# Optimization experiments

Hardware: AMD Instinct MI355X
Metric: run time of the kernel (lower is better)

## Reference

```python
import jax, jax.numpy as jnp
import numpy as np

EPS = 1e-5

def binarize(x):
    # sign binarization with straight-through estimator (matches .data replacement in torch BNN code)
    s = jnp.where(x >= 0, 1.0, -1.0).astype(x.dtype)
    return x + jax.lax.stop_gradient(s - x)

def conv3x3(x, w):
    return jax.lax.conv_general_dilated(x, w, (1, 1), ((1, 1), (1, 1)),
                                        dimension_numbers=('NCHW', 'OIHW', 'NCHW'))

def bn4(x, g, b, m, v):
    inv = jax.lax.rsqrt(v + EPS)
    return (x - m[None, :, None, None]) * (g * inv)[None, :, None, None] + b[None, :, None, None]

def bn2(x, g, b, m, v):
    return (x - m) * (g * jax.lax.rsqrt(v + EPS)) + b

def maxpool2(x):
    return jax.lax.reduce_window(x, -jnp.inf, jax.lax.max, (1, 1, 2, 2), (1, 1, 2, 2), 'VALID')

def ht(x):
    return jnp.clip(x, -1.0, 1.0)


def setup_inputs() -> dict:
    key = jax.random.key(0)
    ks = iter(jax.random.split(key, 64))
    d = {}
    d['x'] = jax.random.normal(next(ks), (256, 3, 32, 32), jnp.float32)
    conv_shapes = [(128, 3), (128, 128), (256, 128), (256, 256), (512, 256), (512, 512)]
    for i, (co, ci) in enumerate(conv_shapes, start=1):
        d[f'w{i}'] = jax.random.normal(next(ks), (co, ci, 3, 3), jnp.float32) * 0.05
        d[f'g{i}'] = jax.random.uniform(next(ks), (co,), jnp.float32, 0.5, 1.5)
        d[f'b{i}'] = jax.random.normal(next(ks), (co,), jnp.float32) * 0.1
        d[f'm{i}'] = jax.random.normal(next(ks), (co,), jnp.float32) * 0.1
        d[f'v{i}'] = jax.random.uniform(next(ks), (co,), jnp.float32, 0.5, 1.5)
    d['bias2'] = jax.random.normal(next(ks), (128,), jnp.float32) * 0.1  # conv2 has default bias=True
    fc_shapes = [(1024, 512 * 4 * 4), (1024, 1024), (10, 1024)]
    for j, (co, ci) in enumerate(fc_shapes, start=7):
        d[f'w{j}'] = jax.random.normal(next(ks), (co, ci), jnp.float32) * 0.02
        d[f'm{j}'] = jax.random.normal(next(ks), (co,), jnp.float32) * 0.1
        d[f'v{j}'] = jax.random.uniform(next(ks), (co,), jnp.float32, 0.5, 1.5)
        if j < 9:  # last BN is affine=False
            d[f'g{j}'] = jax.random.uniform(next(ks), (co,), jnp.float32, 0.5, 1.5)
            d[f'b{j}'] = jax.random.normal(next(ks), (co,), jnp.float32) * 0.1
    return d


def reference(x, w1, g1, b1, m1, v1, w2, bias2, g2, b2, m2, v2, w3, g3, b3, m3, v3,
              w4, g4, b4, m4, v4, w5, g5, b5, m5, v5, w6, g6, b6, m6, v6,
              w7, g7, b7, m7, v7, w8, g8, b8, m8, v8, w9, m9, v9):
    # features
    h = conv3x3(x, binarize(w1))                      # first layer: input NOT binarized (3 channels)
    h = ht(bn4(h, g1, b1, m1, v1))
    h = conv3x3(binarize(h), binarize(w2)) + bias2[None, :, None, None]
    h = ht(bn4(maxpool2(h), g2, b2, m2, v2))
    h = conv3x3(binarize(h), binarize(w3))
    h = ht(bn4(h, g3, b3, m3, v3))
    h = conv3x3(binarize(h), binarize(w4))
    h = ht(bn4(maxpool2(h), g4, b4, m4, v4))
    h = conv3x3(binarize(h), binarize(w5))
    h = ht(bn4(h, g5, b5, m5, v5))
    h = conv3x3(binarize(h), binarize(w6))
    h = ht(bn4(maxpool2(h), g6, b6, m6, v6))          # [B, 512, 4, 4]
    # classifier
    h = h.reshape(-1, 512 * 4 * 4)
    h = ht(bn2(binarize(h) @ binarize(w7).T, g7, b7, m7, v7))
    h = ht(bn2(binarize(h) @ binarize(w8).T, g8, b8, m8, v8))
    h = binarize(h) @ binarize(w9).T
    h = (h - m9) * jax.lax.rsqrt(v9 + EPS)            # BatchNorm1d(affine=False)
    return jax.nn.log_softmax(h, axis=-1)
```

## Files before the change

kernel.cpp:

```cpp
#include <hip/hip_runtime.h>
#include <stdint.h>

typedef unsigned long long u64;

static __device__ __forceinline__ int uread(int v) { return __builtin_amdgcn_readfirstlane(v); }
static __device__ __forceinline__ float fr(float x) { __asm__ volatile("" : "+v"(x)); return x; }

static __device__ __forceinline__ bool bn_neg(float x, float g, float b, float m, float v) {
    float inv = fr(1.0f / fr(sqrtf(fr(v + 1e-5f))));
    float si  = fr(g * inv);
    float t1  = fr(x - m);
    float t2  = fr(t1 * si);
    float bn  = fr(t2 + b);
    return bn < 0.0f;
}


__global__ __launch_bounds__(256) void packw1_kernel(const float* __restrict__ w, float* __restrict__ ws) {
    int id = blockIdx.x * 256 + threadIdx.x;
    if (id >= 27 * 128) return;
    int co = id & 127, j = id >> 7;
    ws[j * 128 + co] = (w[co * 27 + j] < 0.f) ? -1.f : 1.f;
}

__global__ __launch_bounds__(256) void packw_conv2_kernel(const float* __restrict__ w, u64* __restrict__ wb,
                                                          int CINW, int COUT) {
    int wv = blockIdx.x * 4 + (threadIdx.x >> 6);
    if (wv >= COUT * CINW) return;
    int lane = threadIdx.x & 63;
    int wrd = wv % CINW, co = wv / CINW;
    int CIN = CINW * 64;
    const float* p = w + ((size_t)co * CIN + (size_t)wrd * 64 + lane) * 9;
    float f[9];
#pragma unroll
    for (int t = 0; t < 9; ++t) f[t] = p[t];
#pragma unroll
    for (int t = 0; t < 9; ++t) {
        u64 bits = __ballot(f[t] < 0.f);
        if (lane == 0) wb[(size_t)(t * CINW + wrd) * COUT + co] = bits;
    }
}

__global__ __launch_bounds__(256) void packw7_kernel(const float* __restrict__ w, u64* __restrict__ wb) {
    int wv = blockIdx.x * 4 + (threadIdx.x >> 6);
    if (wv >= 1024 * 8) return;
    int lane = threadIdx.x & 63;
    int cw = wv & 7, o = wv >> 3;
    const float* p = w + (size_t)o * 8192 + (size_t)(cw * 64 + lane) * 16;
    float f[16];
#pragma unroll
    for (int i = 0; i < 16; i += 4) {
        float4 q = *(const float4*)(p + i);
        f[i] = q.x; f[i + 1] = q.y; f[i + 2] = q.z; f[i + 3] = q.w;
    }
#pragma unroll
    for (int pixel = 0; pixel < 16; ++pixel) {
        u64 bits = __ballot(f[pixel] < 0.f);
        if (lane == 0) wb[(size_t)(pixel * 8 + cw) * 1024 + o] = bits;
    }
}

__global__ __launch_bounds__(256) void packw8_kernel(const float* __restrict__ w, u64* __restrict__ wb) {
    int wv = blockIdx.x * 4 + (threadIdx.x >> 6);
    if (wv >= 1024 * 16) return;
    int lane = threadIdx.x & 63;
    int k = wv & 15, o = wv >> 4;
    float f = w[(size_t)o * 1024 + k * 64 + lane];
    u64 bits = __ballot(f < 0.f);
    if (lane == 0) wb[(size_t)k * 1024 + o] = bits;
}

__global__ __launch_bounds__(256) void packw9_kernel(const float* __restrict__ w, u64* __restrict__ wb) {
    int wv = blockIdx.x * 4 + (threadIdx.x >> 6);
    if (wv >= 160) return;
    int lane = threadIdx.x & 63;
    int k = wv & 15, o = wv >> 4;
    float f = w[(size_t)o * 1024 + k * 64 + lane];
    u64 bits = __ballot(f < 0.f);
    if (lane == 0) wb[k * 16 + o] = bits;
}

__global__ __launch_bounds__(256, 4) void conv1_kernel(
    const float* __restrict__ x, const float* __restrict__ w1s,
    const float* __restrict__ g, const float* __restrict__ bb,
    const float* __restrict__ m, const float* __restrict__ v,
    u64* __restrict__ out, int N)
{
    int lane = threadIdx.x & 63;
    int rid = uread(blockIdx.x * 4 + (threadIdx.x >> 6));
    if (rid >= N * 32) return;
    int n = rid >> 5, y = rid & 31;
    const float* xb = x + (size_t)n * 3072;
    const bool rv0 = (y > 0), rv2 = (y < 31);
    const int y0 = rv0 ? y - 1 : 0, y2 = rv2 ? y + 1 : 31;

    int co0 = lane, co1 = 64 + lane;
    float w0[27], w1[27];
#pragma unroll
    for (int j = 0; j < 27; ++j) {
        w0[j] = fr(w1s[j * 128 + co0]);
        w1[j] = fr(w1s[j * 128 + co1]);
    }
    float g0 = g[co0], b0 = bb[co0], m0 = m[co0], v0 = v[co0];
    float g1 = g[co1], b1 = bb[co1], m1 = m[co1], v1 = v[co1];

    float cm[9], cc[9], cn[9];
#pragma unroll
    for (int t = 0; t < 9; ++t) cm[t] = 0.f;

    auto ldcol = [&](float* c, int xs) {
#pragma unroll
        for (int ci = 0; ci < 3; ++ci) {
            float a0 = xb[ci * 1024 + y0 * 32 + xs];
            float a1 = xb[ci * 1024 + y  * 32 + xs];
            float a2 = xb[ci * 1024 + y2 * 32 + xs];
            c[0 + ci] = fr(rv0 ? a0 : 0.f);
            c[3 + ci] = fr(a1);
            c[6 + ci] = fr(rv2 ? a2 : 0.f);
        }
    };
    ldcol(cc, 0);

    u64* orow = out + (((size_t)n * 32 + y) * 32) * 2;

    for (int xx = 0; xx < 32; ++xx) {
        if (xx < 31) ldcol(cn, xx + 1);
        else {
#pragma unroll
            for (int t = 0; t < 9; ++t) cn[t] = 0.f;
        }
        float a0 = 0.f, a1 = 0.f;
#pragma unroll
        for (int ky = 0; ky < 3; ++ky) {
#pragma unroll
            for (int ci = 0; ci < 3; ++ci) a0 = fmaf(w0[ci * 9 + ky * 3 + 0], cm[ky * 3 + ci], a0);
#pragma unroll
            for (int ci = 0; ci < 3; ++ci) a0 = fmaf(w0[ci * 9 + ky * 3 + 1], cc[ky * 3 + ci], a0);
#pragma unroll
            for (int ci = 0; ci < 3; ++ci) a0 = fmaf(w0[ci * 9 + ky * 3 + 2], cn[ky * 3 + ci], a0);
        }
#pragma unroll
        for (int ky = 0; ky < 3; ++ky) {
#pragma unroll
            for (int ci = 0; ci < 3; ++ci) a1 = fmaf(w1[ci * 9 + ky * 3 + 0], cm[ky * 3 + ci], a1);
#pragma unroll
            for (int ci = 0; ci < 3; ++ci) a1 = fmaf(w1[ci * 9 + ky * 3 + 1], cc[ky * 3 + ci], a1);
#pragma unroll
            for (int ci = 0; ci < 3; ++ci) a1 = fmaf(w1[ci * 9 + ky * 3 + 2], cn[ky * 3 + ci], a1);
        }
        u64 bits0 = __ballot(bn_neg(a0, g0, b0, m0, v0));
        u64 bits1 = __ballot(bn_neg(a1, g1, b1, m1, v1));
        if (lane == 0) {
            ulonglong2 st; st.x = bits0; st.y = bits1;
            *(ulonglong2*)(orow + xx * 2) = st;
        }
#pragma unroll
        for (int t = 0; t < 9; ++t) { cm[t] = cc[t]; cc[t] = cn[t]; }
    }
}

template<int WORDS, int COW, bool POOL, bool HAS_BIAS, int H, int YS, int MINW>
__global__ __launch_bounds__(256, MINW) void binconv_lds(
    const u64* __restrict__ a, const u64* __restrict__ wb,
    const float* __restrict__ g, const float* __restrict__ bb,
    const float* __restrict__ m, const float* __restrict__ v,
    const float* __restrict__ bias, u64* __restrict__ out, int N)
{
    const int W = H;
    const int OH = POOL ? H / 2 : H, OW = POOL ? W / 2 : W;
    const int COUT = COW * 64;
    const int OROWS = OH / YS;
    const int RMAX = POOL ? OROWS * 2 + 2 : OROWS + 2;
    const int PR = POOL ? 4 : 3;
    const int NW = POOL ? 4 : 1;
    const int W2 = WORDS / 2;
    const int S = POOL ? 2 : 1;
    const int NBC = 9 * WORDS * 64;

    __shared__ alignas(16) u64 tile[RMAX * W * WORDS];

    int blk = blockIdx.x;
    int ys = blk % YS, n = blk / YS;
    int oy0 = ys * OROWS;
    int iy0 = (POOL ? oy0 * 2 - 1 : oy0 - 1); if (iy0 < 0) iy0 = 0;
    int iy1 = (POOL ? (oy0 + OROWS - 1) * 2 + 2 : oy0 + OROWS); if (iy1 > H - 1) iy1 = H - 1;
    int R = iy1 - iy0 + 1;
    {
        const u64* src = a + ((size_t)(n * H + iy0) * W) * WORDS;
        int tot = R * W * WORDS;
        for (int i = threadIdx.x; i < tot; i += 256) tile[i] = src[i];
    }
    __syncthreads();

    int lane = threadIdx.x & 63;
    int wv = uread((int)(threadIdx.x >> 6));

    int cw0, r0, r1;
    if (COW >= 4) { cw0 = wv; r0 = 0; r1 = OROWS; }
    else { cw0 = wv % COW; int chunk = OROWS * COW / 4; r0 = (wv / COW) * chunk; r1 = r0 + chunk; }

    const ulonglong2* t2 = (const ulonglong2*)tile;

    for (int cw = cw0; cw < COW; cw += 4) {
        int co = cw * 64 + lane;
        u64 wgt[9 * WORDS];
#pragma unroll
        for (int t = 0; t < 9 * WORDS; ++t) wgt[t] = wb[(size_t)t * COUT + co];
        float gc = g[co], bc = bb[co], mc = m[co], vc = v[co];
        float bi = HAS_BIAS ? bias[co] : 0.f;

        auto store_px = [&](int oy, int ox, int best) {
            float tv = (float)best;
            if (HAS_BIAS) tv = fr(tv + bi);
            u64 bits = __ballot(bn_neg(tv, gc, bc, mc, vc));
            if (lane == 0) out[((size_t)(n * OH + oy) * OW + ox) * COW + cw] = bits;
        };

        auto px_general = [&](int oy, int ox) {
            int y0 = (POOL ? oy * 2 : oy) - 1;
            bool rv[PR];
#pragma unroll
            for (int p = 0; p < PR; ++p) rv[p] = ((unsigned)(y0 + p) < (unsigned)H);
            int x0 = (POOL ? ox * 2 : ox) - 1;
            bool cv[PR];
#pragma unroll
            for (int q = 0; q < PR; ++q) cv[q] = ((unsigned)(x0 + q) < (unsigned)W);

            int acc[NW], nb[NW];
#pragma unroll
            for (int i = 0; i < NW; ++i) { acc[i] = 0; nb[i] = 0; }
#pragma unroll
            for (int sy = 0; sy < (POOL ? 2 : 1); ++sy)
#pragma unroll
            for (int sx = 0; sx < (POOL ? 2 : 1); ++sx)
#pragma unroll
            for (int ky = 0; ky < 3; ++ky)
#pragma unroll
            for (int kx = 0; kx < 3; ++kx)
                if (rv[sy + ky] && cv[sx + kx]) nb[POOL ? sy * 2 + sx : 0] += WORDS * 64;

#pragma unroll
            for (int w2 = 0; w2 < W2; ++w2) {
                ulonglong2 pt[PR][PR];
#pragma unroll
                for (int p = 0; p < PR; ++p) if (rv[p]) {
                    int lrow = y0 + p - iy0;
#pragma unroll
                    for (int q = 0; q < PR; ++q) if (cv[q])
                        pt[p][q] = t2[(lrow * W + (x0 + q)) * W2 + w2];
                }
#pragma unroll
                for (int sy = 0; sy < (POOL ? 2 : 1); ++sy)
#pragma unroll
                for (int sx = 0; sx < (POOL ? 2 : 1); ++sx)
#pragma unroll
                for (int ky = 0; ky < 3; ++ky)
#pragma unroll
                for (int kx = 0; kx < 3; ++kx)
                    if (rv[sy + ky] && cv[sx + kx]) {
                        ulonglong2 q = pt[sy + ky][sx + kx];
                        int wi = POOL ? sy * 2 + sx : 0;
                        acc[wi] += __popcll(q.x ^ wgt[(ky * 3 + kx) * WORDS + 2 * w2])
                                 + __popcll(q.y ^ wgt[(ky * 3 + kx) * WORDS + 2 * w2 + 1]);
                    }
            }
            int best = 0;
#pragma unroll
            for (int i = 0; i < NW; ++i) {
                int dot = nb[i] - 2 * acc[i];
                best = (i == 0) ? dot : max(best, dot);
            }
            store_px(oy, ox, best);
        };

        for (int oy = oy0 + r0; oy < oy0 + r1; ++oy) {
            int y0 = (POOL ? oy * 2 : oy) - 1;
            if (y0 < 0 || y0 + PR > H) {
                for (int ox = 0; ox < OW; ++ox) px_general(oy, ox);
                continue;
            }
            int base = y0 - iy0;
            px_general(oy, 0);
            if constexpr (W2 == 1) {
                ulonglong2 win[PR][PR];
                const int xl = POOL ? 1 : 0;
#pragma unroll
                for (int p = 0; p < PR; ++p)
#pragma unroll
                    for (int q = 0; q < PR; ++q)
                        win[p][q] = t2[(base + p) * W + xl + q];
                for (int ox = 1; ox < OW - 1; ++ox) {
                    int acc[NW];
#pragma unroll
                    for (int i = 0; i < NW; ++i) acc[i] = 0;
#pragma unroll
                    for (int sy = 0; sy < (POOL ? 2 : 1); ++sy)
#pragma unroll
                    for (int sx = 0; sx < (POOL ? 2 : 1); ++sx)
#pragma unroll
                    for (int ky = 0; ky < 3; ++ky)
#pragma unroll
                    for (int kx = 0; kx < 3; ++kx) {
                        ulonglong2 q = win[sy + ky][sx + kx];
                        int wi = POOL ? sy * 2 + sx : 0;
                        acc[wi] += __popcll(q.x ^ wgt[(ky * 3 + kx) * WORDS])
                                 + __popcll(q.y ^ wgt[(ky * 3 + kx) * WORDS + 1]);
                    }
                    int best = 0;
#pragma unroll
                    for (int i = 0; i < NW; ++i) {
                        int dot = NBC - 2 * acc[i];
                        best = (i == 0) ? dot : max(best, dot);
                    }
                    store_px(oy, ox, best);
                    if (ox < OW - 2) {
                        int xnew = (POOL ? ox * 2 - 1 : ox - 1) + PR;
#pragma unroll
                        for (int p = 0; p < PR; ++p) {
#pragma unroll
                            for (int q = 0; q < PR - S; ++q) win[p][q] = win[p][q + S];
#pragma unroll
                            for (int s = 0; s < S; ++s)
                                win[p][PR - S + s] = t2[(base + p) * W + xnew + s];
                        }
                    }
                }
            } else {
                for (int ox = 1; ox < OW - 1; ++ox) {
                    int x0 = (POOL ? ox * 2 : ox) - 1;
                    int acc[NW];
#pragma unroll
                    for (int i = 0; i < NW; ++i) acc[i] = 0;
#pragma unroll
                    for (int w2 = 0; w2 < W2; ++w2) {
                        ulonglong2 pt[PR][PR];
#pragma unroll
                        for (int p = 0; p < PR; ++p)
#pragma unroll
                            for (int q = 0; q < PR; ++q)
                                pt[p][q] = t2[((base + p) * W + (x0 + q)) * W2 + w2];
#pragma unroll
                        for (int sy = 0; sy < (POOL ? 2 : 1); ++sy)
#pragma unroll
                        for (int sx = 0; sx < (POOL ? 2 : 1); ++sx)
#pragma unroll
                        for (int ky = 0; ky < 3; ++ky)
#pragma unroll
                        for (int kx = 0; kx < 3; ++kx) {
                            ulonglong2 q = pt[sy + ky][sx + kx];
                            int wi = POOL ? sy * 2 + sx : 0;
                            acc[wi] += __popcll(q.x ^ wgt[(ky * 3 + kx) * WORDS + 2 * w2])
                                     + __popcll(q.y ^ wgt[(ky * 3 + kx) * WORDS + 2 * w2 + 1]);
                        }
                    }
                    int best = 0;
#pragma unroll
                    for (int i = 0; i < NW; ++i) {
                        int dot = NBC - 2 * acc[i];
                        best = (i == 0) ? dot : max(best, dot);
                    }
                    store_px(oy, ox, best);
                }
            }
            px_general(oy, OW - 1);
        }
    }
}

template<int KW, int OWRD>
__global__ __launch_bounds__(256) void binfc_kernel(
    const u64* __restrict__ a, const u64* __restrict__ wb,
    const float* __restrict__ g, const float* __restrict__ bb,
    const float* __restrict__ m, const float* __restrict__ v,
    u64* __restrict__ out, int N)
{
    int lane = threadIdx.x & 63;
    int wid = uread(blockIdx.x * 4 + (threadIdx.x >> 6));
    if (wid >= N * OWRD) return;
    int ow = wid & (OWRD - 1), n = wid / OWRD;
    int o = ow * 64 + lane;
    const u64* ap = a + (size_t)n * KW;
    int acc = 0;
#pragma unroll 8
    for (int k = 0; k < KW; ++k)
        acc += __popcll(ap[k] ^ wb[(size_t)k * (OWRD * 64) + o]);
    float dotf = (float)(KW * 64 - 2 * acc);
    u64 bits = __ballot(bn_neg(dotf, g[o], bb[o], m[o], v[o]));
    if (lane == 0) out[(size_t)n * OWRD + ow] = bits;
}

__global__ __launch_bounds__(64) void fc9_kernel(
    const u64* __restrict__ a, const u64* __restrict__ wb,
    const float* __restrict__ m, const float* __restrict__ v, float* __restrict__ out)
{
    int n = blockIdx.x, t = threadIdx.x;
    const u64* ap = a + (size_t)n * 16;
    float val = -1e30f;
    if (t < 10) {
        int acc = 0;
#pragma unroll
        for (int k = 0; k < 16; ++k) acc += __popcll(ap[k] ^ wb[k * 16 + t]);
        float dotf = (float)(1024 - 2 * acc);
        float inv = fr(1.0f / fr(sqrtf(fr(v[t] + 1e-5f))));
        float t1  = fr(dotf - m[t]);
        val = fr(t1 * inv);
    }
    float mx = val;
#pragma unroll
    for (int off = 32; off; off >>= 1) mx = fmaxf(mx, __shfl_xor(mx, off));
    float sh = fr(val - mx);
    double e = (t < 10) ? exp((double)sh) : 0.0;
    double sum = e;
#pragma unroll
    for (int off = 32; off; off >>= 1) sum += __shfl_xor(sum, off);
    if (t < 10) out[n * 10 + t] = (float)((double)sh - log(sum));
}

extern "C" void kernel_launch(void* const* d_in, const int* in_sizes, int n_in,
                              void* d_out, int out_size, void* d_ws, size_t ws_size,
                              hipStream_t stream) {
    auto F = [&](int i) { return (const float*)d_in[i]; };
    const float* x  = F(0);
    const float* w1 = F(1);  const float* g1 = F(2);  const float* b1 = F(3);
    const float* m1 = F(4);  const float* v1 = F(5);
    const float* w2 = F(6);  const float* g2 = F(7);  const float* b2 = F(8);
    const float* m2 = F(9);  const float* v2 = F(10);
    const float* w3 = F(11); const float* g3 = F(12); const float* b3 = F(13);
    const float* m3 = F(14); const float* v3 = F(15);
    const float* w4 = F(16); const float* g4 = F(17); const float* b4 = F(18);
    const float* m4 = F(19); const float* v4 = F(20);
    const float* w5 = F(21); const float* g5 = F(22); const float* b5 = F(23);
    const float* m5 = F(24); const float* v5 = F(25);
    const float* w6 = F(26); const float* g6 = F(27); const float* b6 = F(28);
    const float* m6 = F(29); const float* v6 = F(30);
    const float* bias2 = F(31);
    const float* w7 = F(32); const float* m7 = F(33); const float* v7 = F(34);
    const float* g7 = F(35); const float* b7 = F(36);
    const float* w8 = F(37); const float* m8 = F(38); const float* v8 = F(39);
    const float* g8 = F(40); const float* b8 = F(41);
    const float* w9 = F(42); const float* m9 = F(43); const float* v9 = F(44);
    (void)in_sizes; (void)n_in; (void)ws_size;

    const int N = out_size / 10;
    u64* ws = (u64*)d_ws;
    size_t off = 0;
    auto carve = [&](size_t nwords) { u64* p = ws + off; off += nwords; return p; };
    float* w1s = (float*)carve(1728);
    u64* w2p = carve(2304);
    u64* w3p = carve(4608);
    u64* w4p = carve(9216);
    u64* w5p = carve(18432);
    u64* w6p = carve(36864);
    u64* w7p = carve(131072);
    u64* w8p = carve(16384);
    u64* w9p = carve(256);
    u64* a1 = carve((size_t)N * 32 * 32 * 2);
    u64* a2 = carve((size_t)N * 16 * 16 * 2);
    u64* a3 = carve((size_t)N * 16 * 16 * 4);
    u64* a4 = carve((size_t)N * 8 * 8 * 4);
    u64* a5 = carve((size_t)N * 8 * 8 * 8);
    u64* a6 = carve((size_t)N * 16 * 8);
    u64* f7 = carve((size_t)N * 16);
    u64* f8 = carve((size_t)N * 16);

    packw1_kernel<<<(3456 + 255) / 256, 256, 0, stream>>>(w1, w1s);
    packw_conv2_kernel<<<(128 * 2 + 3) / 4, 256, 0, stream>>>(w2, w2p, 2, 128);
    packw_conv2_kernel<<<(256 * 2 + 3) / 4, 256, 0, stream>>>(w3, w3p, 2, 256);
    packw_conv2_kernel<<<(256 * 4 + 3) / 4, 256, 0, stream>>>(w4, w4p, 4, 256);
    packw_conv2_kernel<<<(512 * 4 + 3) / 4, 256, 0, stream>>>(w5, w5p, 4, 512);
    packw_conv2_kernel<<<(512 * 8 + 3) / 4, 256, 0, stream>>>(w6, w6p, 8, 512);
    packw7_kernel<<<(8192 + 3) / 4, 256, 0, stream>>>(w7, w7p);
    packw8_kernel<<<(16384 + 3) / 4, 256, 0, stream>>>(w8, w8p);
    packw9_kernel<<<(160 + 3) / 4, 256, 0, stream>>>(w9, w9p);

    conv1_kernel<<<(N * 32 + 3) / 4, 256, 0, stream>>>(x, w1s, g1, b1, m1, v1, a1, N);

    binconv_lds<2, 2, true, true, 32, 4, 3><<<N * 4, 256, 0, stream>>>(
        a1, w2p, g2, b2, m2, v2, bias2, a2, N);
    binconv_lds<2, 4, false, false, 16, 4, 3><<<N * 4, 256, 0, stream>>>(
        a2, w3p, g3, b3, m3, v3, nullptr, a3, N);
    binconv_lds<4, 4, true, false, 16, 4, 2><<<N * 4, 256, 0, stream>>>(
        a3, w4p, g4, b4, m4, v4, nullptr, a4, N);
    binconv_lds<4, 8, false, false, 8, 4, 2><<<N * 4, 256, 0, stream>>>(
        a4, w5p, g5, b5, m5, v5, nullptr, a5, N);
    binconv_lds<8, 8, true, false, 8, 4, 2><<<N * 4, 256, 0, stream>>>(
        a5, w6p, g6, b6, m6, v6, nullptr, a6, N);

    binfc_kernel<128, 16><<<(N * 16 + 3) / 4, 256, 0, stream>>>(a6, w7p, g7, b7, m7, v7, f7, N);
    binfc_kernel<16, 16><<<(N * 16 + 3) / 4, 256, 0, stream>>>(f7, w8p, g8, b8, m8, v8, f8, N);

    fc9_kernel<<<N, 64, 0, stream>>>(f8, w9p, m9, v9, (float*)d_out);
}
```

Measured before the change: 703.0 us.

## Stream weight chunks per word-pair and reuse sliding windows in wide binconv layers

For the binary conv layers with more than two 64-bit words per pixel, the kernel no longer holds all 9*WORDS weight words in registers. It loops over word pairs, loading 18 weights per chunk and accumulating groups of output pixels along the row with a sliding window loaded from LDS. This lowers register pressure, so the launch-bounds occupancy hint is raised for conv4, conv5 and conv6. The cost is that weights are reloaded from global memory once per pixel group and word pair.

```diff
diff --git a/kernel.cpp b/kernel.cpp
--- a/kernel.cpp
+++ b/kernel.cpp
@@ -176,6 +176,8 @@
     const int W2 = WORDS / 2;
     const int S = POOL ? 2 : 1;
     const int NBC = 9 * WORDS * 64;
+    const int GPX = (OW <= 4) ? OW : ((NW == 4) ? 4 : OW);
+    const int NG = OW / GPX;
 
     __shared__ alignas(16) u64 tile[RMAX * W * WORDS];
 
@@ -203,9 +205,6 @@
 
     for (int cw = cw0; cw < COW; cw += 4) {
         int co = cw * 64 + lane;
-        u64 wgt[9 * WORDS];
-#pragma unroll
-        for (int t = 0; t < 9 * WORDS; ++t) wgt[t] = wb[(size_t)t * COUT + co];
         float gc = g[co], bc = bb[co], mc = m[co], vc = v[co];
         float bi = HAS_BIAS ? bias[co] : 0.f;
 
@@ -216,38 +215,41 @@
             if (lane == 0) out[((size_t)(n * OH + oy) * OW + ox) * COW + cw] = bits;
         };
 
-        auto px_general = [&](int oy, int ox) {
-            int y0 = (POOL ? oy * 2 : oy) - 1;
-            bool rv[PR];
-#pragma unroll
-            for (int p = 0; p < PR; ++p) rv[p] = ((unsigned)(y0 + p) < (unsigned)H);
-            int x0 = (POOL ? ox * 2 : ox) - 1;
-            bool cv[PR];
-#pragma unroll
-            for (int q = 0; q < PR; ++q) cv[q] = ((unsigned)(x0 + q) < (unsigned)W);
-
-            int acc[NW], nb[NW];
-#pragma unroll
-            for (int i = 0; i < NW; ++i) { acc[i] = 0; nb[i] = 0; }
-#pragma unroll
-            for (int sy = 0; sy < (POOL ? 2 : 1); ++sy)
-#pragma unroll
-            for (int sx = 0; sx < (POOL ? 2 : 1); ++sx)
-#pragma unroll
-            for (int ky = 0; ky < 3; ++ky)
-#pragma unroll
-            for (int kx = 0; kx < 3; ++kx)
-                if (rv[sy + ky] && cv[sx + kx]) nb[POOL ? sy * 2 + sx : 0] += WORDS * 64;
-
-#pragma unroll
-            for (int w2 = 0; w2 < W2; ++w2) {
+        if constexpr (W2 == 1) {
+            u64 wgt[18];
+#pragma unroll
+            for (int t = 0; t < 18; ++t) wgt[t] = wb[(size_t)t * COUT + co];
+
+            auto px_general = [&](int oy, int ox) {
+                int y0 = (POOL ? oy * 2 : oy) - 1;
+                bool rv[PR];
+#pragma unroll
+                for (int p = 0; p < PR; ++p) rv[p] = ((unsigned)(y0 + p) < (unsigned)H);
+                int x0 = (POOL ? ox * 2 : ox) - 1;
+                bool cv[PR];
+#pragma unroll
+                for (int q = 0; q < PR; ++q) cv[q] = ((unsigned)(x0 + q) < (unsigned)W);
+
+                int acc[NW], nb[NW];
+#pragma unroll
+                for (int i = 0; i < NW; ++i) { acc[i] = 0; nb[i] = 0; }
+#pragma unroll
+                for (int sy = 0; sy < (POOL ? 2 : 1); ++sy)
+#pragma unroll
+                for (int sx = 0; sx < (POOL ? 2 : 1); ++sx)
+#pragma unroll
+                for (int ky = 0; ky < 3; ++ky)
+#pragma unroll
+                for (int kx = 0; kx < 3; ++kx)
+                    if (rv[sy + ky] && cv[sx + kx]) nb[POOL ? sy * 2 + sx : 0] += WORDS * 64;
+
                 ulonglong2 pt[PR][PR];
 #pragma unroll
                 for (int p = 0; p < PR; ++p) if (rv[p]) {
                     int lrow = y0 + p - iy0;
 #pragma unroll
                     for (int q = 0; q < PR; ++q) if (cv[q])
-                        pt[p][q] = t2[(lrow * W + (x0 + q)) * W2 + w2];
+                        pt[p][q] = t2[(lrow * W + (x0 + q))];
                 }
 #pragma unroll
                 for (int sy = 0; sy < (POOL ? 2 : 1); ++sy)
@@ -260,28 +262,26 @@
                     if (rv[sy + ky] && cv[sx + kx]) {
                         ulonglong2 q = pt[sy + ky][sx + kx];
                         int wi = POOL ? sy * 2 + sx : 0;
-                        acc[wi] += __popcll(q.x ^ wgt[(ky * 3 + kx) * WORDS + 2 * w2])
-                                 + __popcll(q.y ^ wgt[(ky * 3 + kx) * WORDS + 2 * w2 + 1]);
+                        acc[wi] += __popcll(q.x ^ wgt[(ky * 3 + kx) * 2])
+                                 + __popcll(q.y ^ wgt[(ky * 3 + kx) * 2 + 1]);
                     }
-            }
-            int best = 0;
-#pragma unroll
-            for (int i = 0; i < NW; ++i) {
-                int dot = nb[i] - 2 * acc[i];
-                best = (i == 0) ? dot : max(best, dot);
-            }
-            store_px(oy, ox, best);
-        };
-
-        for (int oy = oy0 + r0; oy < oy0 + r1; ++oy) {
-            int y0 = (POOL ? oy * 2 : oy) - 1;
-            if (y0 < 0 || y0 + PR > H) {
-                for (int ox = 0; ox < OW; ++ox) px_general(oy, ox);
-                continue;
-            }
-            int base = y0 - iy0;
-            px_general(oy, 0);
-            if constexpr (W2 == 1) {
+                int best = 0;
+#pragma unroll
+                for (int i = 0; i < NW; ++i) {
+                    int dot = nb[i] - 2 * acc[i];
+                    best = (i == 0) ? dot : max(best, dot);
+                }
+                store_px(oy, ox, best);
+            };
+
+            for (int oy = oy0 + r0; oy < oy0 + r1; ++oy) {
+                int y0 = (POOL ? oy * 2 : oy) - 1;
+                if (y0 < 0 || y0 + PR > H) {
+                    for (int ox = 0; ox < OW; ++ox) px_general(oy, ox);
+                    continue;
+                }
+                int base = y0 - iy0;
+                px_general(oy, 0);
                 ulonglong2 win[PR][PR];
                 const int xl = POOL ? 1 : 0;
 #pragma unroll
@@ -303,8 +303,8 @@
                     for (int kx = 0; kx < 3; ++kx) {
                         ulonglong2 q = win[sy + ky][sx + kx];
                         int wi = POOL ? sy * 2 + sx : 0;
-                        acc[wi] += __popcll(q.x ^ wgt[(ky * 3 + kx) * WORDS])
-                                 + __popcll(q.y ^ wgt[(ky * 3 + kx) * WORDS + 1]);
+                        acc[wi] += __popcll(q.x ^ wgt[(ky * 3 + kx) * 2])
+                                 + __popcll(q.y ^ wgt[(ky * 3 + kx) * 2 + 1]);
                     }
                     int best = 0;
 #pragma unroll
@@ -325,44 +325,114 @@
                         }
                     }
                 }
-            } else {
-                for (int ox = 1; ox < OW - 1; ++ox) {
-                    int x0 = (POOL ? ox * 2 : ox) - 1;
-                    int acc[NW];
-#pragma unroll
-                    for (int i = 0; i < NW; ++i) acc[i] = 0;
-#pragma unroll
+                px_general(oy, OW - 1);
+            }
+        } else {
+            for (int oy = oy0 + r0; oy < oy0 + r1; ++oy) {
+                int y0r = (POOL ? oy * 2 : oy) - 1;
+                bool rv[PR];
+#pragma unroll
+                for (int p = 0; p < PR; ++p) rv[p] = ((unsigned)(y0r + p) < (unsigned)H);
+                int baseR = y0r - iy0;
+
+#pragma unroll
+                for (int gg = 0; gg < NG; ++gg) {
+                    int acc[GPX][NW];
+#pragma unroll
+                    for (int i = 0; i < GPX; ++i)
+#pragma unroll
+                        for (int wi = 0; wi < NW; ++wi) acc[i][wi] = 0;
+
+#pragma unroll 1
                     for (int w2 = 0; w2 < W2; ++w2) {
-                        ulonglong2 pt[PR][PR];
-#pragma unroll
-                        for (int p = 0; p < PR; ++p)
-#pragma unroll
-                            for (int q = 0; q < PR; ++q)
-                                pt[p][q] = t2[((base + p) * W + (x0 + q)) * W2 + w2];
-#pragma unroll
-                        for (int sy = 0; sy < (POOL ? 2 : 1); ++sy)
-#pragma unroll
-                        for (int sx = 0; sx < (POOL ? 2 : 1); ++sx)
-#pragma unroll
-                        for (int ky = 0; ky < 3; ++ky)
-#pragma unroll
-                        for (int kx = 0; kx < 3; ++kx) {
-                            ulonglong2 q = pt[sy + ky][sx + kx];
-                            int wi = POOL ? sy * 2 + sx : 0;
-                            acc[wi] += __popcll(q.x ^ wgt[(ky * 3 + kx) * WORDS + 2 * w2])
-                                     + __popcll(q.y ^ wgt[(ky * 3 + kx) * WORDS + 2 * w2 + 1]);
+                        u64 wc[18];
+#pragma unroll
+                        for (int t = 0; t < 9; ++t) {
+                            wc[t * 2]     = wb[(size_t)(t * WORDS + 2 * w2) * COUT + co];
+                            wc[t * 2 + 1] = wb[(size_t)(t * WORDS + 2 * w2 + 1) * COUT + co];
+                        }
+                        ulonglong2 win[PR][PR];
+#pragma unroll
+                        for (int i = 0; i < GPX; ++i) {
+                            const int ox = gg * GPX + i;
+                            const int x0 = S * ox - 1;
+                            if (i == 0) {
+#pragma unroll
+                                for (int q = 0; q < PR; ++q) {
+                                    const int x = x0 + q;
+                                    if (x >= 0 && x < W) {
+#pragma unroll
+                                        for (int p = 0; p < PR; ++p)
+                                            if (rv[p]) win[p][q] = t2[((baseR + p) * W + x) * W2 + w2];
+                                    }
+                                }
+                            } else {
+#pragma unroll
+                                for (int p = 0; p < PR; ++p)
+#pragma unroll
+                                    for (int q = 0; q < PR - S; ++q) win[p][q] = win[p][q + S];
+#pragma unroll
+                                for (int s = 0; s < S; ++s) {
+                                    const int x = x0 + PR - S + s;
+                                    if (x >= 0 && x < W) {
+#pragma unroll
+                                        for (int p = 0; p < PR; ++p)
+                                            if (rv[p]) win[p][PR - S + s] = t2[((baseR + p) * W + x) * W2 + w2];
+                                    }
+                                }
+                            }
+#pragma unroll
+                            for (int sy = 0; sy < (POOL ? 2 : 1); ++sy)
+#pragma unroll
+                            for (int sx = 0; sx < (POOL ? 2 : 1); ++sx)
+#pragma unroll
+                            for (int ky = 0; ky < 3; ++ky)
+#pragma unroll
+                            for (int kx = 0; kx < 3; ++kx) {
+                                const int xq = x0 + sx + kx;
+                                if (xq >= 0 && xq < W) {
+                                    if (rv[sy + ky]) {
+                                        ulonglong2 q = win[sy + ky][sx + kx];
+                                        const int t = ky * 3 + kx;
+                                        const int wi = POOL ? sy * 2 + sx : 0;
+                                        acc[i][wi] += __popcll(q.x ^ wc[t * 2])
+                                                    + __popcll(q.y ^ wc[t * 2 + 1]);
+                                    }
+                                }
+                            }
                         }
                     }
-                    int best = 0;
-#pragma unroll
-                    for (int i = 0; i < NW; ++i) {
-                        int dot = NBC - 2 * acc[i];
-                        best = (i == 0) ? dot : max(best, dot);
+
+#pragma unroll
+                    for (int i = 0; i < GPX; ++i) {
+                        const int ox = gg * GPX + i;
+                        const int x0 = S * ox - 1;
+                        int nb[NW];
+#pragma unroll
+                        for (int wi = 0; wi < NW; ++wi) nb[wi] = 0;
+#pragma unroll
+                        for (int sy = 0; sy < (POOL ? 2 : 1); ++sy)
+#pragma unroll
+                        for (int sx = 0; sx < (POOL ? 2 : 1); ++sx)
+#pragma unroll
+                        for (int ky = 0; ky < 3; ++ky)
+#pragma unroll
+                        for (int kx = 0; kx < 3; ++kx) {
+                            const int xq = x0 + sx + kx;
+                            if (xq >= 0 && xq < W) {
+                                if (rv[sy + ky]) nb[POOL ? sy * 2 + sx : 0] += WORDS * 64;
+                            }
+                        }
+                        int best = 0;
+#pragma unroll
+                        for (int wi = 0; wi < NW; ++wi) {
+                            int dot = nb[wi] - 2 * acc[i][wi];
+                            best = (wi == 0) ? dot : max(best, dot);
+                        }
+                        store_px(oy, ox, best);
                     }
-                    store_px(oy, ox, best);
                 }
             }
-            px_general(oy, OW - 1);
         }
     }
 }
@@ -479,11 +549,11 @@
         a1, w2p, g2, b2, m2, v2, bias2, a2, N);
     binconv_lds<2, 4, false, false, 16, 4, 3><<<N * 4, 256, 0, stream>>>(
         a2, w3p, g3, b3, m3, v3, nullptr, a3, N);
-    binconv_lds<4, 4, true, false, 16, 4, 2><<<N * 4, 256, 0, stream>>>(
+    binconv_lds<4, 4, true, false, 16, 4, 3><<<N * 4, 256, 0, stream>>>(
         a3, w4p, g4, b4, m4, v4, nullptr, a4, N);
-    binconv_lds<4, 8, false, false, 8, 4, 2><<<N * 4, 256, 0, stream>>>(
+    binconv_lds<4, 8, false, false, 8, 4, 4><<<N * 4, 256, 0, stream>>>(
         a4, w5p, g5, b5, m5, v5, nullptr, a5, N);
-    binconv_lds<8, 8, true, false, 8, 4, 2><<<N * 4, 256, 0, stream>>>(
+    binconv_lds<8, 8, true, false, 8, 4, 4><<<N * 4, 256, 0, stream>>>(
         a5, w6p, g6, b6, m6, v6, nullptr, a6, N);
 
     binfc_kernel<128, 16><<<(N * 16 + 3) / 4, 256, 0, stream>>>(a6, w7p, g7, b7, m7, v7, f7, N);
```

Result: faster. 680.3 us (-3.2%).
